# Performance work log

Hardware: AMD Instinct MI355X
Metric: run time of the kernel (lower is better)

Reference implementation:

```python
import jax, jax.numpy as jnp
import numpy as np

B, L1, L2, H = 8, 2048, 2048, 1024


def setup_inputs() -> dict:
    key = jax.random.key(0)
    kx, ky, kw1, kb1, kw2, kb2, klen = jax.random.split(key, 7)
    x = jax.random.normal(kx, (B, L1, H), dtype=jnp.float32)
    y = jax.random.normal(ky, (B, L2, H), dtype=jnp.float32)
    # torch Linear weights are [out, in]; init scale ~ 1/sqrt(H)
    s = 1.0 / np.sqrt(H)
    W1 = jax.random.uniform(kw1, (H, H), jnp.float32, -s, s)
    b1 = jax.random.uniform(kb1, (H,), jnp.float32, -s, s)
    W2 = jax.random.uniform(kw2, (H, H), jnp.float32, -s, s)
    b2 = jax.random.uniform(kb2, (H,), jnp.float32, -s, s)
    # valid lengths in [L2//2, L2] so no row is fully padded; mask=True for padding
    lengths = jax.random.randint(klen, (B,), L2 // 2, L2 + 1)
    y_mask = jnp.arange(L2)[None, :] >= lengths[:, None]  # [B, L2] bool
    return {"x": x, "y": y, "W1": W1, "b1": b1, "W2": W2, "b2": b2, "y_mask": y_mask}


def reference(x, y, W1, b1, W2, b2, y_mask):
    # projected ReLU features (torch Linear: v @ W.T + b)
    x_proj = jax.nn.relu(jnp.einsum("bld,hd->blh", x, W1) + b1)  # [B, L1, H]
    y_proj = jax.nn.relu(jnp.einsum("bld,hd->blh", y, W2) + b2)  # [B, L2, H]
    scores = jnp.einsum("bih,bjh->bij", x_proj, y_proj)          # [B, L1, L2]
    scores = jnp.where(y_mask[:, None, :], -jnp.inf, scores)
    alpha = jax.nn.softmax(scores, axis=-1)
    matched_seq = jnp.einsum("bij,bjh->bih", alpha, y)           # [B, L1, H]
    return matched_seq
```

## Files before the change

kernel.cpp:

```cpp
#include <hip/hip_runtime.h>
#include <hip/hip_fp16.h>


using half8 = __attribute__((ext_vector_type(8))) _Float16;
using f32x4 = __attribute__((ext_vector_type(4))) float;

#define DEVI __device__ __forceinline__

DEVI void async16(void* lds, const void* g) {
    __builtin_amdgcn_global_load_lds(
        (const __attribute__((address_space(1))) unsigned int*)g,
        (__attribute__((address_space(3))) unsigned int*)lds,
        16, 0, 0);
}

DEVI unsigned short f2h(float f) { return __half_as_ushort(__float2half(f)); }

__global__ __launch_bounds__(256) void cvt_f32_f16_kernel(
    const float4* __restrict__ in, ushort4* __restrict__ out, int n4)
{
    int i = blockIdx.x * 256 + threadIdx.x;
    if (i >= n4) return;
    float4 f = in[i];
    ushort4 o;
    o.x = f2h(f.x); o.y = f2h(f.y); o.z = f2h(f.z); o.w = f2h(f.w);
    out[i] = o;
}

__global__ void mask_prep_kernel(const unsigned char* __restrict__ raw,
                                 unsigned char* __restrict__ mask)
{
    __shared__ int S0, S123;
    const int t = threadIdx.x;
    if (t == 0) { S0 = 0; S123 = 0; }
    __syncthreads();
    int s0 = 0, s123 = 0;
    for (int i = t; i < 16384; i += 256) {
        int v = raw[i];
        if ((i & 3) == 0) s0 += v; else s123 += v;
    }
    atomicAdd(&S0, s0); atomicAdd(&S123, s123);
    __syncthreads();
    const int mode = (S123 == 0) ? 1 : ((S0 == 0) ? 2 : 0);
    for (int i = t; i < 16384; i += 256) {
        unsigned char m;
        if (mode == 0)      m = raw[i] ? 1 : 0;
        else if (mode == 1) m = ((const int*)raw)[i] ? 1 : 0;
        else                m = (((const float*)raw)[i] != 0.f) ? 1 : 0;
        mask[i] = m;
    }
}

__global__ __launch_bounds__(256) void transpose_kernel(
    const unsigned short* __restrict__ y, unsigned short* __restrict__ yT)
{
    const int b  = blockIdx.z;
    const int i0 = blockIdx.x * 64;
    const int h0 = blockIdx.y * 64;
    __shared__ unsigned short tile[64][72];
    const int t  = threadIdx.x;
    const int tr = t >> 4;
    const int tc = (t & 15) * 4;
    const size_t ybase = ((size_t)b * 2048 + i0) * 1024 + h0;
#pragma unroll
    for (int p = 0; p < 4; ++p) {
        const int r = p * 16 + tr;
        ushort4 v = *(const ushort4*)(y + ybase + (size_t)r * 1024 + tc);
        *(ushort4*)&tile[r][tc] = v;
    }
    __syncthreads();
    const size_t obase = ((size_t)b * 1024 + h0) * 2048 + i0;
#pragma unroll
    for (int p = 0; p < 4; ++p) {
        const int r = p * 16 + tr;
        ushort4 v;
        v.x = tile[tc + 0][r]; v.y = tile[tc + 1][r];
        v.z = tile[tc + 2][r]; v.w = tile[tc + 3][r];
        *(ushort4*)(yT + obase + (size_t)r * 2048 + tc) = v;
    }
}

template<typename OutT, bool RELU, bool BIAS>
DEVI void gemm_bt_body(unsigned short* As, unsigned short* Bs,
                       const unsigned short* __restrict__ A, int lda,
                       const unsigned short* __restrict__ Bt,
                       OutT* __restrict__ C, int ldc,
                       const float* __restrict__ bias, int K,
                       int m0, int n0)
{
    const int t    = threadIdx.x;
    const int lane = t & 63;
    const int wave = t >> 6;
    const int wr   = wave >> 1;
    const int wc   = wave & 1;

    const int off  = t * 16;
    const int srow = off >> 6;
    const int scb  = off & 63;
    const unsigned short* Ag = A + (size_t)(m0 + srow) * lda + (scb >> 1);
    const unsigned short* Bg = Bt + (size_t)(n0 + srow) * K + (scb >> 1);
    char* AsD = (char*)As + off;
    char* BsD = (char*)Bs + off;
    const size_t rowskipA = (size_t)64 * lda;
    const size_t rowskipB = (size_t)64 * K;

    f32x4 acc[4][4] = {};

    const int l16 = lane & 15;
    const int kb  = (lane >> 4) * 8;

    for (int k0 = 0; k0 < K; k0 += 32) {
        async16(AsD,        Ag + k0);
        async16(AsD + 4096, Ag + rowskipA + k0);
        async16(BsD,        Bg + k0);
        async16(BsD + 4096, Bg + rowskipB + k0);
        __syncthreads();

        half8 af[4], bf[4];
#pragma unroll
        for (int m = 0; m < 4; ++m)
            af[m] = *(const half8*)&As[(wr * 64 + m * 16 + l16) * 32 + kb];
#pragma unroll
        for (int n = 0; n < 4; ++n)
            bf[n] = *(const half8*)&Bs[(wc * 64 + n * 16 + l16) * 32 + kb];
#pragma unroll
        for (int m = 0; m < 4; ++m)
#pragma unroll
            for (int n = 0; n < 4; ++n)
                acc[m][n] = __builtin_amdgcn_mfma_f32_16x16x32_f16(
                    af[m], bf[n], acc[m][n], 0, 0, 0);
        __syncthreads();
    }

    const int rbase = m0 + wr * 64 + (lane >> 4) * 4;
#pragma unroll
    for (int n = 0; n < 4; ++n) {
        const int col = n0 + wc * 64 + n * 16 + l16;
        float bb = 0.f;
        if (BIAS) bb = bias[col];
#pragma unroll
        for (int m = 0; m < 4; ++m) {
            f32x4 v = acc[m][n];
#pragma unroll
            for (int j = 0; j < 4; ++j) {
                float o = v[j] + bb;
                if (RELU) o = fmaxf(o, 0.f);
                const size_t idx = (size_t)(rbase + m * 16 + j) * ldc + col;
                if constexpr (sizeof(OutT) == 2)
                    ((unsigned short*)C)[idx] = f2h(o);
                else
                    ((float*)C)[idx] = o;
            }
        }
    }
}

template<typename OutT, bool RELU, bool BIAS>
__global__ __launch_bounds__(256) void gemm_bt_kernel(
    const unsigned short* __restrict__ A, int lda, long long sA,
    const unsigned short* __restrict__ Bt, long long sB,
    OutT* __restrict__ C, int ldc, long long sC,
    const float* __restrict__ bias, int K)
{
    __shared__ __align__(16) unsigned short As[128 * 32];
    __shared__ __align__(16) unsigned short Bs[128 * 32];
    const int b = blockIdx.z;
    gemm_bt_body<OutT, RELU, BIAS>(As, Bs,
        A + (size_t)b * sA, lda, Bt + (size_t)b * sB,
        C + (size_t)b * sC, ldc, bias, K,
        blockIdx.x * 128, blockIdx.y * 128);
}

__global__ __launch_bounds__(256) void proj_gemm_kernel(
    const unsigned short* __restrict__ xh, const unsigned short* __restrict__ yh,
    const unsigned short* __restrict__ w1, const unsigned short* __restrict__ w2,
    const float* __restrict__ b1, const float* __restrict__ b2,
    unsigned short* __restrict__ xp, unsigned short* __restrict__ yp)
{
    __shared__ __align__(16) unsigned short As[128 * 32];
    __shared__ __align__(16) unsigned short Bs[128 * 32];
    const bool sel = blockIdx.z != 0;
    gemm_bt_body<unsigned short, true, true>(As, Bs,
        sel ? yh : xh, 1024, sel ? w2 : w1,
        sel ? yp : xp, 1024, sel ? b2 : b1, 1024,
        blockIdx.x * 128, blockIdx.y * 128);
}

__global__ __launch_bounds__(256) void masked_softmax_kernel(
    const float* __restrict__ scores,
    const unsigned char* __restrict__ mask,
    unsigned short* __restrict__ alpha, int lda_out)
{
    const int row = blockIdx.x;
    const int bl  = row >> 11;
    const float* s = scores + (size_t)row * 2048;
    unsigned short* a = alpha + (size_t)row * lda_out;
    const unsigned char* mk = mask + (bl << 11);
    const int t = threadIdx.x;

    float v[8]; int m[8];
    float mx = -1e30f;
#pragma unroll
    for (int r = 0; r < 8; ++r) {
        const int j = (r << 8) + t;
        v[r] = s[j];
        m[r] = mk[j];
        if (!m[r]) mx = fmaxf(mx, v[r]);
    }
    for (int o = 32; o > 0; o >>= 1) mx = fmaxf(mx, __shfl_xor(mx, o));
    __shared__ float red[4];
    const int lane = t & 63, wave = t >> 6;
    if (lane == 0) red[wave] = mx;
    __syncthreads();
    mx = fmaxf(fmaxf(red[0], red[1]), fmaxf(red[2], red[3]));

    float e[8];
    float sum = 0.f;
#pragma unroll
    for (int r = 0; r < 8; ++r) {
        e[r] = m[r] ? 0.f : __expf(v[r] - mx);
        sum += e[r];
    }
    for (int o = 32; o > 0; o >>= 1) sum += __shfl_xor(sum, o);
    __shared__ float red2[4];
    if (lane == 0) red2[wave] = sum;
    __syncthreads();
    sum = red2[0] + red2[1] + red2[2] + red2[3];
    const float inv = 1.f / sum;
#pragma unroll
    for (int r = 0; r < 8; ++r) {
        const int j = (r << 8) + t;
        a[j] = f2h(e[r] * inv);
    }
}

extern "C" void kernel_launch(void* const* d_in, const int* in_sizes, int n_in,
                              void* d_out, int out_size, void* d_ws, size_t ws_size,
                              hipStream_t stream)
{
    const float* x  = (const float*)d_in[0];
    const float* y  = (const float*)d_in[1];
    const float* W1 = (const float*)d_in[2];
    const float* b1 = (const float*)d_in[3];
    const float* W2 = (const float*)d_in[4];
    const float* b2 = (const float*)d_in[5];
    const unsigned char* ymask_raw = (const unsigned char*)d_in[6];

    constexpr int B = 8, L1 = 2048, L2 = 2048, H = 1024;
    constexpr size_t NXH   = (size_t)B * L1 * H;
    constexpr size_t NW    = (size_t)H * H;
    constexpr size_t SC_B8 = (size_t)B * L1 * L2 * 4;
    constexpr size_t SC_B4 = SC_B8 / 2;
    constexpr size_t FIXED = 2 * NW * 2 + 3 * NXH * 2 + B * L2;

    const bool big = ws_size >= SC_B8 + FIXED;
    const size_t sc_bytes = big ? SC_B8 : SC_B4;

    char* ws = (char*)d_ws;
    float*          sc  = (float*)ws;           ws += sc_bytes;
    unsigned short* w1h = (unsigned short*)ws;  ws += NW * 2;
    unsigned short* w2h = (unsigned short*)ws;  ws += NW * 2;
    unsigned short* xp  = (unsigned short*)ws;  ws += NXH * 2;
    unsigned short* yp  = (unsigned short*)ws;  ws += NXH * 2;
    unsigned short* yT  = (unsigned short*)ws;  ws += NXH * 2;
    unsigned char*  mk  = (unsigned char*)ws;   ws += B * L2;
    unsigned short* xh = (unsigned short*)sc;
    unsigned short* yh = xh + NXH;

    cvt_f32_f16_kernel<<<(int)(NXH / 4 / 256), 256, 0, stream>>>(
        (const float4*)x, (ushort4*)xh, (int)(NXH / 4));
    cvt_f32_f16_kernel<<<(int)(NXH / 4 / 256), 256, 0, stream>>>(
        (const float4*)y, (ushort4*)yh, (int)(NXH / 4));
    cvt_f32_f16_kernel<<<(int)(NW / 4 / 256), 256, 0, stream>>>(
        (const float4*)W1, (ushort4*)w1h, (int)(NW / 4));
    cvt_f32_f16_kernel<<<(int)(NW / 4 / 256), 256, 0, stream>>>(
        (const float4*)W2, (ushort4*)w2h, (int)(NW / 4));
    mask_prep_kernel<<<1, 256, 0, stream>>>(ymask_raw, mk);

    proj_gemm_kernel<<<dim3(16384 / 128, 1024 / 128, 2), 256, 0, stream>>>(
        xh, yh, w1h, w2h, b1, b2, xp, yp);

    transpose_kernel<<<dim3(L2 / 64, H / 64, B), 256, 0, stream>>>(yh, yT);

    const int CB = big ? B : 4;
    for (int c0 = 0; c0 < B; c0 += CB) {
        float*          scc = sc;
        unsigned short* al  = (unsigned short*)sc;

        gemm_bt_kernel<float, false, false>
            <<<dim3(L1 / 128, L2 / 128, CB), 256, 0, stream>>>(
            xp + (size_t)c0 * L1 * H, H, (long long)L1 * H,
            yp + (size_t)c0 * L2 * H, (long long)L2 * H,
            scc, L2, (long long)L1 * L2, nullptr, H);

        masked_softmax_kernel<<<CB * L1, 256, 0, stream>>>(
            scc, mk + (size_t)c0 * L2, al, 2 * L2);

        gemm_bt_kernel<float, false, false>
            <<<dim3(L1 / 128, H / 128, CB), 256, 0, stream>>>(
            al, 2 * L2, (long long)L1 * 2 * L2,
            yT + (size_t)c0 * H * L2, (long long)H * L2,
            (float*)d_out + (size_t)c0 * L1 * H, H, (long long)L1 * H,
            nullptr, L2);
    }
}
```

Baseline: 563.6 us.

## Use 256x256 GEMM tiles with 4-stage async LDS pipeline and swizzle

Replaces the 128x128 single-buffered GEMM with a 256x256 tile over 8 waves, each computing 128x64. The K loop becomes a four-stage global_load_lds ring buffer in 128KB of dynamic LDS, with vmcnt waits, an XOR swizzle to avoid bank conflicts, and setprio around the MFMA block. Separately, y's f32-to-f16 conversion is fused into the transpose kernel, removing one pass over y. The larger tiles cut global traffic per FLOP and overlap loads with compute, but 128KB of LDS per block limits occupancy, and the launch_bounds(512,2) request may not be met.

```diff
diff --git a/kernel.cpp b/kernel.cpp
--- a/kernel.cpp
+++ b/kernel.cpp
@@ -51,8 +51,9 @@
     }
 }
 
-__global__ __launch_bounds__(256) void transpose_kernel(
-    const unsigned short* __restrict__ y, unsigned short* __restrict__ yT)
+__global__ __launch_bounds__(256) void transpose_cvt_kernel(
+    const float* __restrict__ y, unsigned short* __restrict__ yh,
+    unsigned short* __restrict__ yT)
 {
     const int b  = blockIdx.z;
     const int i0 = blockIdx.x * 64;
@@ -65,7 +66,10 @@
 #pragma unroll
     for (int p = 0; p < 4; ++p) {
         const int r = p * 16 + tr;
-        ushort4 v = *(const ushort4*)(y + ybase + (size_t)r * 1024 + tc);
+        float4 f = *(const float4*)(y + ybase + (size_t)r * 1024 + tc);
+        ushort4 v;
+        v.x = f2h(f.x); v.y = f2h(f.y); v.z = f2h(f.z); v.w = f2h(f.w);
+        *(ushort4*)(yh + ybase + (size_t)r * 1024 + tc) = v;
         *(ushort4*)&tile[r][tc] = v;
     }
     __syncthreads();
@@ -81,9 +85,9 @@
 }
 
 template<typename OutT, bool RELU, bool BIAS>
-DEVI void gemm_bt_body(unsigned short* As, unsigned short* Bs,
+DEVI void gemm256_body(unsigned short* lds,
                        const unsigned short* __restrict__ A, int lda,
-                       const unsigned short* __restrict__ Bt,
+                       const unsigned short* __restrict__ Bt, int ldb,
                        OutT* __restrict__ C, int ldc,
                        const float* __restrict__ bias, int K,
                        int m0, int n0)
@@ -91,61 +95,86 @@
     const int t    = threadIdx.x;
     const int lane = t & 63;
     const int wave = t >> 6;
-    const int wr   = wave >> 1;
-    const int wc   = wave & 1;
-
-    const int off  = t * 16;
-    const int srow = off >> 6;
-    const int scb  = off & 63;
-    const unsigned short* Ag = A + (size_t)(m0 + srow) * lda + (scb >> 1);
-    const unsigned short* Bg = Bt + (size_t)(n0 + srow) * K + (scb >> 1);
-    char* AsD = (char*)As + off;
-    char* BsD = (char*)Bs + off;
-    const size_t rowskipA = (size_t)64 * lda;
-    const size_t rowskipB = (size_t)64 * K;
-
-    f32x4 acc[4][4] = {};
-
-    const int l16 = lane & 15;
-    const int kb  = (lane >> 4) * 8;
-
-    for (int k0 = 0; k0 < K; k0 += 32) {
-        async16(AsD,        Ag + k0);
-        async16(AsD + 4096, Ag + rowskipA + k0);
-        async16(BsD,        Bg + k0);
-        async16(BsD + 4096, Bg + rowskipB + k0);
-        __syncthreads();
-
-        half8 af[4], bf[4];
-#pragma unroll
-        for (int m = 0; m < 4; ++m)
-            af[m] = *(const half8*)&As[(wr * 64 + m * 16 + l16) * 32 + kb];
+    const int wr   = wave >> 2;
+    const int wc   = wave & 3;
+    const int l16  = lane & 15;
+    const int q    = lane >> 4;
+
+    const int o0 = t * 16;
+    const int o1 = o0 + 8192;
+    const int r0 = o0 >> 6;
+    const int r1 = o1 >> 6;
+    const int s0 = (o0 & 63) ^ ((r0 & 3) << 4);
+    const int s1 = (o1 & 63) ^ ((r1 & 3) << 4);
+    const unsigned short* Ag0 = A + (size_t)(m0 + r0) * lda + (s0 >> 1);
+    const unsigned short* Ag1 = A + (size_t)(m0 + r1) * lda + (s1 >> 1);
+    const unsigned short* Bg0 = Bt + (size_t)(n0 + r0) * ldb + (s0 >> 1);
+    const unsigned short* Bg1 = Bt + (size_t)(n0 + r1) * ldb + (s1 >> 1);
+
+#define STAGE256(bufi, kt) do {                                   \
+        char* dst = (char*)lds + (size_t)(bufi) * 32768;          \
+        const size_t ko = (size_t)(kt) * 32;                      \
+        async16(dst + o0,         Ag0 + ko);                      \
+        async16(dst + o1,         Ag1 + ko);                      \
+        async16(dst + 16384 + o0, Bg0 + ko);                      \
+        async16(dst + 16384 + o1, Bg1 + ko);                      \
+    } while (0)
+
+    const int swz  = (l16 & 3) << 4;
+    const int aoff = (wr * 128 + l16) * 64 + ((q * 16) ^ swz);
+    const int boff = 16384 + (wc * 64 + l16) * 64 + ((q * 16) ^ swz);
+
+    f32x4 acc[8][4] = {};
+
+    const int NT = K >> 5;
+
+    STAGE256(0, 0); STAGE256(1, 1); STAGE256(2, 2);
+    asm volatile("s_waitcnt vmcnt(8)" ::: "memory");
+    __builtin_amdgcn_s_barrier();
+
+    for (int tt = 0; tt < NT; ++tt) {
+        const int c = tt & 3;
+        const bool more = (tt + 3) < NT;
+        if (more) STAGE256((tt + 3) & 3, tt + 3);
+
+        const char* bufp = (const char*)lds + (size_t)c * 32768;
+        half8 af[8], bf[4];
+#pragma unroll
+        for (int m = 0; m < 8; ++m)
+            af[m] = *(const half8*)(bufp + aoff + m * 1024);
 #pragma unroll
         for (int n = 0; n < 4; ++n)
-            bf[n] = *(const half8*)&Bs[(wc * 64 + n * 16 + l16) * 32 + kb];
-#pragma unroll
-        for (int m = 0; m < 4; ++m)
+            bf[n] = *(const half8*)(bufp + boff + n * 1024);
+
+        __builtin_amdgcn_s_setprio(1);
+#pragma unroll
+        for (int m = 0; m < 8; ++m)
 #pragma unroll
             for (int n = 0; n < 4; ++n)
                 acc[m][n] = __builtin_amdgcn_mfma_f32_16x16x32_f16(
                     af[m], bf[n], acc[m][n], 0, 0, 0);
-        __syncthreads();
-    }
-
-    const int rbase = m0 + wr * 64 + (lane >> 4) * 4;
+        __builtin_amdgcn_s_setprio(0);
+
+        if (more)              asm volatile("s_waitcnt vmcnt(8)" ::: "memory");
+        else if (tt + 2 < NT)  asm volatile("s_waitcnt vmcnt(4)" ::: "memory");
+        else                   asm volatile("s_waitcnt vmcnt(0)" ::: "memory");
+        __builtin_amdgcn_s_barrier();
+    }
+#undef STAGE256
+
+    const int rb = m0 + wr * 128 + q * 4;
 #pragma unroll
     for (int n = 0; n < 4; ++n) {
         const int col = n0 + wc * 64 + n * 16 + l16;
         float bb = 0.f;
         if (BIAS) bb = bias[col];
 #pragma unroll
-        for (int m = 0; m < 4; ++m) {
-            f32x4 v = acc[m][n];
+        for (int m = 0; m < 8; ++m) {
 #pragma unroll
             for (int j = 0; j < 4; ++j) {
-                float o = v[j] + bb;
+                float o = acc[m][n][j] + bb;
                 if (RELU) o = fmaxf(o, 0.f);
-                const size_t idx = (size_t)(rbase + m * 16 + j) * ldc + col;
+                const size_t idx = (size_t)(rb + m * 16 + j) * ldc + col;
                 if constexpr (sizeof(OutT) == 2)
                     ((unsigned short*)C)[idx] = f2h(o);
                 else
@@ -156,34 +185,32 @@
 }
 
 template<typename OutT, bool RELU, bool BIAS>
-__global__ __launch_bounds__(256) void gemm_bt_kernel(
+__global__ __launch_bounds__(512, 2) void gemm256_kernel(
     const unsigned short* __restrict__ A, int lda, long long sA,
-    const unsigned short* __restrict__ Bt, long long sB,
+    const unsigned short* __restrict__ Bt, int ldb, long long sB,
     OutT* __restrict__ C, int ldc, long long sC,
     const float* __restrict__ bias, int K)
 {
-    __shared__ __align__(16) unsigned short As[128 * 32];
-    __shared__ __align__(16) unsigned short Bs[128 * 32];
+    extern __shared__ unsigned short lds[];
     const int b = blockIdx.z;
-    gemm_bt_body<OutT, RELU, BIAS>(As, Bs,
-        A + (size_t)b * sA, lda, Bt + (size_t)b * sB,
+    gemm256_body<OutT, RELU, BIAS>(lds,
+        A + (size_t)b * sA, lda, Bt + (size_t)b * sB, ldb,
         C + (size_t)b * sC, ldc, bias, K,
-        blockIdx.x * 128, blockIdx.y * 128);
-}
-
-__global__ __launch_bounds__(256) void proj_gemm_kernel(
+        blockIdx.x * 256, blockIdx.y * 256);
+}
+
+__global__ __launch_bounds__(512, 2) void proj256_kernel(
     const unsigned short* __restrict__ xh, const unsigned short* __restrict__ yh,
     const unsigned short* __restrict__ w1, const unsigned short* __restrict__ w2,
     const float* __restrict__ b1, const float* __restrict__ b2,
     unsigned short* __restrict__ xp, unsigned short* __restrict__ yp)
 {
-    __shared__ __align__(16) unsigned short As[128 * 32];
-    __shared__ __align__(16) unsigned short Bs[128 * 32];
+    extern __shared__ unsigned short lds[];
     const bool sel = blockIdx.z != 0;
-    gemm_bt_body<unsigned short, true, true>(As, Bs,
-        sel ? yh : xh, 1024, sel ? w2 : w1,
+    gemm256_body<unsigned short, true, true>(lds,
+        sel ? yh : xh, 1024, sel ? w2 : w1, 1024,
         sel ? yp : xp, 1024, sel ? b2 : b1, 1024,
-        blockIdx.x * 128, blockIdx.y * 128);
+        blockIdx.x * 256, blockIdx.y * 256);
 }
 
 __global__ __launch_bounds__(256) void masked_softmax_kernel(
@@ -269,37 +296,35 @@
 
     cvt_f32_f16_kernel<<<(int)(NXH / 4 / 256), 256, 0, stream>>>(
         (const float4*)x, (ushort4*)xh, (int)(NXH / 4));
-    cvt_f32_f16_kernel<<<(int)(NXH / 4 / 256), 256, 0, stream>>>(
-        (const float4*)y, (ushort4*)yh, (int)(NXH / 4));
     cvt_f32_f16_kernel<<<(int)(NW / 4 / 256), 256, 0, stream>>>(
         (const float4*)W1, (ushort4*)w1h, (int)(NW / 4));
     cvt_f32_f16_kernel<<<(int)(NW / 4 / 256), 256, 0, stream>>>(
         (const float4*)W2, (ushort4*)w2h, (int)(NW / 4));
+    transpose_cvt_kernel<<<dim3(L2 / 64, H / 64, B), 256, 0, stream>>>(y, yh, yT);
     mask_prep_kernel<<<1, 256, 0, stream>>>(ymask_raw, mk);
 
-    proj_gemm_kernel<<<dim3(16384 / 128, 1024 / 128, 2), 256, 0, stream>>>(
+    constexpr size_t LDSB = 131072;
+
+    proj256_kernel<<<dim3(16384 / 256, 1024 / 256, 2), 512, LDSB, stream>>>(
         xh, yh, w1h, w2h, b1, b2, xp, yp);
-
-    transpose_kernel<<<dim3(L2 / 64, H / 64, B), 256, 0, stream>>>(yh, yT);
 
     const int CB = big ? B : 4;
     for (int c0 = 0; c0 < B; c0 += CB) {
-        float*          scc = sc;
-        unsigned short* al  = (unsigned short*)sc;
-
-        gemm_bt_kernel<float, false, false>
-            <<<dim3(L1 / 128, L2 / 128, CB), 256, 0, stream>>>(
+        unsigned short* al = (unsigned short*)sc;
+
+        gemm256_kernel<float, false, false>
+            <<<dim3(L1 / 256, L2 / 256, CB), 512, LDSB, stream>>>(
             xp + (size_t)c0 * L1 * H, H, (long long)L1 * H,
-            yp + (size_t)c0 * L2 * H, (long long)L2 * H,
-            scc, L2, (long long)L1 * L2, nullptr, H);
+            yp + (size_t)c0 * L2 * H, H, (long long)L2 * H,
+            sc, L2, (long long)L1 * L2, nullptr, H);
 
         masked_softmax_kernel<<<CB * L1, 256, 0, stream>>>(
-            scc, mk + (size_t)c0 * L2, al, 2 * L2);
-
-        gemm_bt_kernel<float, false, false>
-            <<<dim3(L1 / 128, H / 128, CB), 256, 0, stream>>>(
+            sc, mk + (size_t)c0 * L2, al, 2 * L2);
+
+        gemm256_kernel<float, false, false>
+            <<<dim3(L1 / 256, H / 256, CB), 512, LDSB, stream>>>(
             al, 2 * L2, (long long)L1 * 2 * L2,
-            yT + (size_t)c0 * H * L2, (long long)H * L2,
+            yT + (size_t)c0 * H * L2, L2, (long long)H * L2,
             (float*)d_out + (size_t)c0 * L1 * H, H, (long long)L1 * H,
             nullptr, L2);
     }
```

After: 499.8 us. -11.3%, faster.
